# Kernel tuning notes

Measured on AMD Instinct MI355X. Metric: run time of the kernel, lower is better.

Reference implementation:

```python
import jax, jax.numpy as jnp
import numpy as np

# ---- JPEG constants ----
_Y_TABLE = np.array([
    [16, 11, 10, 16, 24, 40, 51, 61],
    [12, 12, 14, 19, 26, 58, 60, 55],
    [14, 13, 16, 24, 40, 57, 69, 56],
    [14, 17, 22, 29, 51, 87, 80, 62],
    [18, 22, 37, 56, 68, 109, 103, 77],
    [24, 35, 55, 64, 81, 104, 113, 92],
    [49, 64, 78, 87, 103, 121, 120, 101],
    [72, 92, 95, 98, 112, 100, 103, 99]], dtype=np.float32)
_C_TABLE = np.full((8, 8), 99.0, dtype=np.float32)
_C_TABLE[:4, :4] = np.array([
    [17, 18, 24, 47],
    [18, 21, 26, 66],
    [24, 26, 56, 99],
    [47, 66, 99, 99]], dtype=np.float32)

_i = np.arange(8, dtype=np.float64)
_T = (np.cos((2 * _i[:, None, None, None] + 1) * _i[None, None, :, None] * np.pi / 16)
      * np.cos((2 * _i[None, :, None, None] + 1) * _i[None, None, None, :] * np.pi / 16))
_alpha = np.ones(8); _alpha[0] = 1.0 / np.sqrt(2.0)
DCT_T = jnp.asarray(_T, jnp.float32)
DCT_SCALE = jnp.asarray(np.outer(_alpha, _alpha) * 0.25, jnp.float32)
IDCT_ALPHA = jnp.asarray(np.outer(_alpha, _alpha), jnp.float32)
Y_T = jnp.asarray(_Y_TABLE)
C_T = jnp.asarray(_C_TABLE)


def _split_blocks(c):
    # [N,H,W] -> [N, (H//8)*(W//8), 8, 8]
    N, H, W = c.shape
    return c.reshape(N, H // 8, 8, W // 8, 8).transpose(0, 1, 3, 2, 4).reshape(N, -1, 8, 8)


def _merge_blocks(b, H, W):
    N = b.shape[0]
    return b.reshape(N, H // 8, W // 8, 8, 8).transpose(0, 1, 3, 2, 4).reshape(N, H, W)


def _dct8x8(b):
    return DCT_SCALE * jnp.einsum('nbxy,xyuv->nbuv', b - 128.0, DCT_T)


def _idct8x8(b):
    return 0.25 * jnp.einsum('nbuv,xyuv->nbxy', b * IDCT_ALPHA, DCT_T) + 128.0


def _diff_round(x):
    r = jnp.round(x)
    return r + (x - r) ** 3


def _quality_to_factor(q):
    return (5000.0 / q if q < 50 else 200.0 - 2.0 * q) / 100.0


def _diff_jpeg(x, quality=99.0):
    # x: [N,3,16,16] roughly in [0,1]
    factor = _quality_to_factor(quality)
    img = x * 255.0
    M = jnp.array([[0.299, 0.587, 0.114],
                   [-0.168736, -0.331264, 0.5],
                   [0.5, -0.418688, -0.081312]], jnp.float32)
    shift = jnp.array([0.0, 128.0, 128.0], jnp.float32)
    ycc = jnp.einsum('nchw,kc->nkhw', img, M) + shift[None, :, None, None]
    y, cb, cr = ycc[:, 0], ycc[:, 1], ycc[:, 2]
    N, H, W = y.shape
    sub = lambda c: c.reshape(N, H // 2, 2, W // 2, 2).mean(axis=(2, 4))  # 2x2 chroma subsample

    def codec(c, tab):
        q = _diff_round(_dct8x8(_split_blocks(c)) / (tab * factor))
        return _idct8x8(q * (tab * factor))

    y2 = _merge_blocks(codec(y, Y_T), H, W)
    up = lambda c: jnp.repeat(jnp.repeat(c, 2, axis=1), 2, axis=2)
    cb2 = up(_merge_blocks(codec(sub(cb), C_T), H // 2, W // 2))
    cr2 = up(_merge_blocks(codec(sub(cr), C_T), H // 2, W // 2))
    ycc2 = jnp.stack([y2, cb2, cr2], axis=1)
    Mi = jnp.array([[1.0, 0.0, 1.402],
                    [1.0, -0.344136, -0.714136],
                    [1.0, 1.772, 0.0]], jnp.float32)
    shift2 = jnp.array([0.0, -128.0, -128.0], jnp.float32)
    rgb = jnp.einsum('nkhw,ck->nchw', ycc2 + shift2[None, :, None, None], Mi)
    return jnp.clip(rgb, 0.0, 255.0) / 255.0


def setup_inputs() -> dict:
    key = jax.random.key(0)
    x = jax.random.normal(key, (32, 1024, 14, 14), dtype=jnp.float32)
    return {"x": x}


def reference(x):
    orig_min = jnp.min(x, axis=(-2, -1), keepdims=True)
    orig_max = jnp.max(x, axis=(-2, -1), keepdims=True)
    rng = orig_max - orig_min + 1e-5
    xn = (x - orig_min) / rng
    B, C, H, W = x.shape
    # replicate each channel into a 3-channel image
    xr = jnp.broadcast_to(xn[:, :, None], (B, C, 3, H, W)).reshape(B * C, 3, H, W)
    xp = jnp.pad(xr, ((0, 0), (0, 0), (1, 1), (1, 1)), mode='edge')  # 14x14 -> 16x16
    comp = _diff_jpeg(xp, 99.0)
    comp = comp[:, :, 1:-1, 1:-1].reshape(B, C, 3, H, W).mean(axis=2)
    return comp * rng + orig_min
```

## Files before the change

kernel.cpp:

```cpp
#include <hip/hip_runtime.h>


namespace {

constexpr int CH_PER_WG = 8;
constexpr int HW        = 196;
constexpr int CS        = 288;

constexpr float CM[8][8] = {
  { 0.35355339059327376f,  0.35355339059327376f,  0.35355339059327376f,  0.35355339059327376f,
    0.35355339059327376f,  0.35355339059327376f,  0.35355339059327376f,  0.35355339059327376f},
  { 0.49039264020161522f,  0.41573480615127262f,  0.27778511650980114f,  0.09754516100806417f,
   -0.09754516100806417f, -0.27778511650980114f, -0.41573480615127262f, -0.49039264020161522f},
  { 0.46193976625564337f,  0.19134171618254492f, -0.19134171618254492f, -0.46193976625564337f,
   -0.46193976625564337f, -0.19134171618254492f,  0.19134171618254492f,  0.46193976625564337f},
  { 0.41573480615127262f, -0.09754516100806417f, -0.49039264020161522f, -0.27778511650980114f,
    0.27778511650980114f,  0.49039264020161522f,  0.09754516100806417f, -0.41573480615127262f},
  { 0.35355339059327376f, -0.35355339059327376f, -0.35355339059327376f,  0.35355339059327376f,
    0.35355339059327376f, -0.35355339059327376f, -0.35355339059327376f,  0.35355339059327376f},
  { 0.27778511650980114f, -0.49039264020161522f,  0.09754516100806417f,  0.41573480615127262f,
   -0.41573480615127262f, -0.09754516100806417f,  0.49039264020161522f, -0.27778511650980114f},
  { 0.19134171618254492f, -0.46193976625564337f,  0.46193976625564337f, -0.19134171618254492f,
   -0.19134171618254492f,  0.46193976625564337f, -0.46193976625564337f,  0.19134171618254492f},
  { 0.09754516100806417f, -0.27778511650980114f,  0.41573480615127262f, -0.49039264020161522f,
    0.49039264020161522f, -0.41573480615127262f,  0.27778511650980114f, -0.09754516100806417f},
};

}

__device__ const float YQTAB[8][8] = {
  {16,11,10,16,24,40,51,61},
  {12,12,14,19,26,58,60,55},
  {14,13,16,24,40,57,69,56},
  {14,17,22,29,51,87,80,62},
  {18,22,37,56,68,109,103,77},
  {24,35,55,64,81,104,113,92},
  {49,64,78,87,103,121,120,101},
  {72,92,95,98,112,100,103,99},
};

#define WAVE_LDS_SYNC() asm volatile("s_waitcnt lgkmcnt(0)" ::: "memory")

__global__ __launch_bounds__(256)
void jpeg_codec_kernel(const float* __restrict__ x, float* __restrict__ out) {
  __shared__ __align__(16) float s_raw[CH_PER_WG * HW];
  __shared__ float s_bufA[CH_PER_WG * CS];
  __shared__ float s_bufB[CH_PER_WG * CS];
  __shared__ float s_min[CH_PER_WG];
  __shared__ float s_scale[CH_PER_WG];

  const int tid = threadIdx.x;
  const long long base = (long long)blockIdx.x * (CH_PER_WG * HW);

  {
    const float4* x4 = (const float4*)(x + base);
    float4* r4 = (float4*)s_raw;
    r4[tid & 255] = x4[tid & 255];
    int t = tid + 256;
    if (t < (CH_PER_WG * HW) / 4) r4[t] = x4[t];
  }
  __syncthreads();

  const int ch = tid >> 5;
  const int l  = tid & 31;

  float mn, inv;
  {
    float vmin = 1e30f, vmax = -1e30f;
    const float4* c4 = (const float4*)(s_raw + ch * HW);
    {
      float4 v = c4[l];
      vmin = fminf(fminf(vmin, v.x), fminf(v.y, fminf(v.z, v.w)));
      vmax = fmaxf(fmaxf(vmax, v.x), fmaxf(v.y, fmaxf(v.z, v.w)));
    }
    if (l < 17) {
      float4 v = c4[l + 32];
      vmin = fminf(fminf(vmin, v.x), fminf(v.y, fminf(v.z, v.w)));
      vmax = fmaxf(fmaxf(vmax, v.x), fmaxf(v.y, fmaxf(v.z, v.w)));
    }
    #pragma unroll
    for (int off = 16; off; off >>= 1) {
      vmin = fminf(vmin, __shfl_xor(vmin, off, 64));
      vmax = fmaxf(vmax, __shfl_xor(vmax, off, 64));
    }
    mn = vmin;
    float rng = vmax - vmin + 1e-5f;
    inv = 255.0f / rng;
    if (l == 0) { s_min[ch] = mn; s_scale[ch] = rng * (1.0f / 255.0f); }
  }

  const int b = l >> 3;
  const int i = l & 7;
  const int rbase = ch * CS + b * 72 + i * 9;
  const int wbase = ch * CS + b * 72 + i;

  float m[8];

  {
    const int pr = ((b >> 1) << 3) + i;
    int sr = pr - 1; sr = sr < 0 ? 0 : (sr > 13 ? 13 : sr);
    const float* rp = s_raw + ch * HW + sr * 14;
    #pragma unroll
    for (int j = 0; j < 8; ++j) {
      int pc = ((b & 1) << 3) + j - 1; pc = pc < 0 ? 0 : (pc > 13 ? 13 : pc);
      m[j] = fmaf(rp[pc] - mn, inv, -128.0f);
    }
    #pragma unroll
    for (int k = 0; k < 8; ++k) {
      float s = 0.0f;
      #pragma unroll
      for (int j = 0; j < 8; ++j) s = fmaf(m[j], CM[k][j], s);
      s_bufB[wbase + 9 * k] = s;
    }
  }
  WAVE_LDS_SYNC();

  #pragma unroll
  for (int j = 0; j < 8; ++j) m[j] = s_bufB[rbase + j];
  #pragma unroll
  for (int k = 0; k < 8; ++k) {
    float s = 0.0f;
    #pragma unroll
    for (int j = 0; j < 8; ++j) s = fmaf(m[j], CM[k][j], s);
    float qv = YQTAB[k][i] * 0.02f;
    float xq = s / qv;
    float r  = rintf(xq);
    float e  = xq - r;
    s_bufA[wbase + 9 * k] = (r + e * e * e) * qv;
  }
  WAVE_LDS_SYNC();

  #pragma unroll
  for (int j = 0; j < 8; ++j) m[j] = s_bufA[rbase + j];
  #pragma unroll
  for (int k = 0; k < 8; ++k) {
    float s = 0.0f;
    #pragma unroll
    for (int j = 0; j < 8; ++j) s = fmaf(m[j], CM[j][k], s);
    s_bufB[wbase + 9 * k] = s;
  }
  WAVE_LDS_SYNC();

  #pragma unroll
  for (int j = 0; j < 8; ++j) m[j] = s_bufB[rbase + j];
  #pragma unroll
  for (int k = 0; k < 8; ++k) {
    float s = 0.0f;
    #pragma unroll
    for (int j = 0; j < 8; ++j) s = fmaf(m[j], CM[j][k], s);
    s_bufA[wbase + 9 * k] = s;
  }
  __syncthreads();

  {
    float4* o4 = (float4*)(out + base);
    #pragma unroll
    for (int k = 0; k < 2; ++k) {
      int t = tid + k * 256;
      if (t < (CH_PER_WG * HW) / 4) {
        int idx = 4 * t;
        int c2  = idx / HW;
        int rem = idx - c2 * HW;
        int r0  = rem / 14, c0 = rem - 14 * r0;
        float cmn = s_min[c2], cscale = s_scale[c2];
        float vals[4];
        #pragma unroll
        for (int q = 0; q < 4; ++q) {
          int rr = r0, cc = c0 + q;
          if (cc >= 14) { cc -= 14; ++rr; }
          int pr = rr + 1, pc = cc + 1;
          int bb = ((pr >> 3) << 1) | (pc >> 3);
          float v = s_bufA[c2 * CS + bb * 72 + (pr & 7) * 9 + (pc & 7)] + 128.0f;
          v = v < 0.0f ? 0.0f : (v > 255.0f ? 255.0f : v);
          vals[q] = fmaf(v, cscale, cmn);
        }
        o4[t] = make_float4(vals[0], vals[1], vals[2], vals[3]);
      }
    }
  }
}

extern "C" void kernel_launch(void* const* d_in, const int* in_sizes, int n_in,
                              void* d_out, int out_size, void* d_ws, size_t ws_size,
                              hipStream_t stream) {
  const float* x = (const float*)d_in[0];
  float* out     = (float*)d_out;
  const int ntot = in_sizes[0];
  const int nch  = ntot / HW;
  const int grid = (nch + CH_PER_WG - 1) / CH_PER_WG;
  hipLaunchKernelGGL(jpeg_codec_kernel, dim3(grid), dim3(256), 0, stream,
                     x, out);
}
```

Measured before the change: 84.29 us.

## Give each wave its own channels, load via global_load_lds, drop block barriers

Each 64-lane wave now owns two channels end to end. Input is copied straight from global memory into LDS with the gfx950 global_load_lds builtin, and the wave waits on vmcnt instead of a block-wide __syncthreads. Per-channel min and scale now travel by wave shuffles instead of shared variables. The separate raw staging buffer is gone: raw data is placed in the first ping-pong buffer, which cuts LDS per block and may allow more resident blocks. The design depends on wave-lockstep ordering between reading the raw data and overwriting that same LDS region, and on the direct-to-LDS load being supported and correctly aligned.

```diff
diff --git a/kernel.cpp b/kernel.cpp
--- a/kernel.cpp
+++ b/kernel.cpp
@@ -6,6 +6,7 @@
 constexpr int CH_PER_WG = 8;
 constexpr int HW        = 196;
 constexpr int CS        = 288;
+constexpr int WREG      = 2 * CS;
 
 constexpr float CM[8][8] = {
   { 0.35355339059327376f,  0.35355339059327376f,  0.35355339059327376f,  0.35355339059327376f,
@@ -40,34 +41,41 @@
 };
 
 #define WAVE_LDS_SYNC() asm volatile("s_waitcnt lgkmcnt(0)" ::: "memory")
+#define WAVE_VM_SYNC()  asm volatile("s_waitcnt vmcnt(0)" ::: "memory")
+
+typedef __attribute__((address_space(1))) const void gvoid_t;
+typedef __attribute__((address_space(3))) void       lvoid_t;
 
 __global__ __launch_bounds__(256)
 void jpeg_codec_kernel(const float* __restrict__ x, float* __restrict__ out) {
-  __shared__ __align__(16) float s_raw[CH_PER_WG * HW];
-  __shared__ float s_bufA[CH_PER_WG * CS];
-  __shared__ float s_bufB[CH_PER_WG * CS];
-  __shared__ float s_min[CH_PER_WG];
-  __shared__ float s_scale[CH_PER_WG];
+  __shared__ __align__(16) float s_A[CH_PER_WG * CS];
+  __shared__ __align__(16) float s_B[CH_PER_WG * CS];
 
   const int tid = threadIdx.x;
-  const long long base = (long long)blockIdx.x * (CH_PER_WG * HW);
-
-  {
-    const float4* x4 = (const float4*)(x + base);
-    float4* r4 = (float4*)s_raw;
-    r4[tid & 255] = x4[tid & 255];
-    int t = tid + 256;
-    if (t < (CH_PER_WG * HW) / 4) r4[t] = x4[t];
-  }
-  __syncthreads();
-
-  const int ch = tid >> 5;
-  const int l  = tid & 31;
+  const int w   = tid >> 6;
+  const int wl  = tid & 63;
+  const int chl = (tid >> 5) & 1;
+  const int l   = tid & 31;
+
+  const long long g4 = (long long)blockIdx.x * (CH_PER_WG * HW / 4) + w * (2 * HW / 4);
+
+  {
+    const float4* x4 = (const float4*)x + g4;
+    float* raw = s_A + w * WREG;
+    __builtin_amdgcn_global_load_lds((gvoid_t*)(x4 + wl), (lvoid_t*)raw, 16, 0, 0);
+    if (wl < 2 * HW / 4 - 64)
+      __builtin_amdgcn_global_load_lds((gvoid_t*)(x4 + 64 + wl),
+                                       (lvoid_t*)(raw + 256), 16, 0, 0);
+  }
+  WAVE_VM_SYNC();
+
+  const float* raw_ch = s_A + w * WREG + chl * HW;
 
   float mn, inv;
+  float mn0, mn1, sc0, sc1;
   {
     float vmin = 1e30f, vmax = -1e30f;
-    const float4* c4 = (const float4*)(s_raw + ch * HW);
+    const float4* c4 = (const float4*)raw_ch;
     {
       float4 v = c4[l];
       vmin = fminf(fminf(vmin, v.x), fminf(v.y, fminf(v.z, v.w)));
@@ -84,22 +92,25 @@
       vmax = fmaxf(vmax, __shfl_xor(vmax, off, 64));
     }
     mn = vmin;
-    float rng = vmax - vmin + 1e-5f;
-    inv = 255.0f / rng;
-    if (l == 0) { s_min[ch] = mn; s_scale[ch] = rng * (1.0f / 255.0f); }
+    float rng   = vmax - vmin + 1e-5f;
+    inv         = 255.0f / rng;
+    float scale = rng * (1.0f / 255.0f);
+    mn0 = __shfl(mn, 0, 64);  mn1 = __shfl(mn, 32, 64);
+    sc0 = __shfl(scale, 0, 64); sc1 = __shfl(scale, 32, 64);
   }
 
   const int b = l >> 3;
   const int i = l & 7;
-  const int rbase = ch * CS + b * 72 + i * 9;
-  const int wbase = ch * CS + b * 72 + i;
+  const int cbase = w * WREG + chl * CS;
+  const int rbase = cbase + b * 72 + i * 9;
+  const int wbase = cbase + b * 72 + i;
 
   float m[8];
 
   {
     const int pr = ((b >> 1) << 3) + i;
     int sr = pr - 1; sr = sr < 0 ? 0 : (sr > 13 ? 13 : sr);
-    const float* rp = s_raw + ch * HW + sr * 14;
+    const float* rp = raw_ch + sr * 14;
     #pragma unroll
     for (int j = 0; j < 8; ++j) {
       int pc = ((b & 1) << 3) + j - 1; pc = pc < 0 ? 0 : (pc > 13 ? 13 : pc);
@@ -110,13 +121,13 @@
       float s = 0.0f;
       #pragma unroll
       for (int j = 0; j < 8; ++j) s = fmaf(m[j], CM[k][j], s);
-      s_bufB[wbase + 9 * k] = s;
-    }
-  }
-  WAVE_LDS_SYNC();
-
-  #pragma unroll
-  for (int j = 0; j < 8; ++j) m[j] = s_bufB[rbase + j];
+      s_B[wbase + 9 * k] = s;
+    }
+  }
+  WAVE_LDS_SYNC();
+
+  #pragma unroll
+  for (int j = 0; j < 8; ++j) m[j] = s_B[rbase + j];
   #pragma unroll
   for (int k = 0; k < 8; ++k) {
     float s = 0.0f;
@@ -126,43 +137,45 @@
     float xq = s / qv;
     float r  = rintf(xq);
     float e  = xq - r;
-    s_bufA[wbase + 9 * k] = (r + e * e * e) * qv;
-  }
-  WAVE_LDS_SYNC();
-
-  #pragma unroll
-  for (int j = 0; j < 8; ++j) m[j] = s_bufA[rbase + j];
+    s_A[wbase + 9 * k] = (r + e * e * e) * qv;
+  }
+  WAVE_LDS_SYNC();
+
+  #pragma unroll
+  for (int j = 0; j < 8; ++j) m[j] = s_A[rbase + j];
   #pragma unroll
   for (int k = 0; k < 8; ++k) {
     float s = 0.0f;
     #pragma unroll
     for (int j = 0; j < 8; ++j) s = fmaf(m[j], CM[j][k], s);
-    s_bufB[wbase + 9 * k] = s;
-  }
-  WAVE_LDS_SYNC();
-
-  #pragma unroll
-  for (int j = 0; j < 8; ++j) m[j] = s_bufB[rbase + j];
+    s_B[wbase + 9 * k] = s;
+  }
+  WAVE_LDS_SYNC();
+
+  #pragma unroll
+  for (int j = 0; j < 8; ++j) m[j] = s_B[rbase + j];
   #pragma unroll
   for (int k = 0; k < 8; ++k) {
     float s = 0.0f;
     #pragma unroll
     for (int j = 0; j < 8; ++j) s = fmaf(m[j], CM[j][k], s);
-    s_bufA[wbase + 9 * k] = s;
-  }
-  __syncthreads();
-
-  {
-    float4* o4 = (float4*)(out + base);
+    s_A[wbase + 9 * k] = s;
+  }
+  WAVE_LDS_SYNC();
+
+  {
+    float4* o4 = (float4*)out + g4;
     #pragma unroll
     for (int k = 0; k < 2; ++k) {
-      int t = tid + k * 256;
-      if (t < (CH_PER_WG * HW) / 4) {
+      int t = wl + k * 64;
+      if (t < 2 * HW / 4) {
         int idx = 4 * t;
-        int c2  = idx / HW;
-        int rem = idx - c2 * HW;
+        int c2l = idx / HW;
+        int rem = idx - c2l * HW;
         int r0  = rem / 14, c0 = rem - 14 * r0;
-        float cmn = s_min[c2], cscale = s_scale[c2];
+        float cmn = c2l ? mn1 : mn0;
+        float csc = c2l ? sc1 : sc0;
+        const float* blk = s_A + w * WREG + c2l * CS;
         float vals[4];
         #pragma unroll
         for (int q = 0; q < 4; ++q) {
@@ -170,9 +183,9 @@
           if (cc >= 14) { cc -= 14; ++rr; }
           int pr = rr + 1, pc = cc + 1;
           int bb = ((pr >> 3) << 1) | (pc >> 3);
-          float v = s_bufA[c2 * CS + bb * 72 + (pr & 7) * 9 + (pc & 7)] + 128.0f;
+          float v = blk[bb * 72 + (pr & 7) * 9 + (pc & 7)] + 128.0f;
           v = v < 0.0f ? 0.0f : (v > 255.0f ? 255.0f : v);
-          vals[q] = fmaf(v, cscale, cmn);
+          vals[q] = fmaf(v, csc, cmn);
         }
         o4[t] = make_float4(vals[0], vals[1], vals[2], vals[3]);
       }
```

After: 83.54 us. No clear change (-0.9%).
